# Performance work log

Hardware: AMD Instinct MI355X
Metric: run time of the kernel (lower is better)

## Reference

```python
import jax, jax.numpy as jnp
import numpy as np

RADIUS = 0.25
NUM_NEIGHBORS = 32
POS_DIM = 24
STEM_C = 64
PATCH_C = 256
LN_EPS = 1e-5


def query_ball_point(radius, nsample, xyz, new_xyz):
    # xyz: [B,N,3], new_xyz: [B,S,3] -> idx [B,S,nsample] (PointNet++ ball query)
    N = xyz.shape[1]
    sqr = (jnp.sum(new_xyz ** 2, -1)[:, :, None]
           + jnp.sum(xyz ** 2, -1)[:, None, :]
           - 2.0 * jnp.einsum('bsd,bnd->bsn', new_xyz, xyz))  # [B,S,N]
    idx = jnp.broadcast_to(jnp.arange(N, dtype=jnp.int32), sqr.shape)
    idx = jnp.where(sqr > radius * radius, N, idx)
    idx = jnp.sort(idx, axis=-1)[..., :nsample]  # first nsample in-ball (by index order)
    first = idx[..., :1]
    idx = jnp.where(idx == N, first, idx)  # pad empty slots with first neighbor
    return idx


def index_points(points, idx):
    # points [B,N,C], idx [B,S,K] -> [B,S,K,C]
    return jax.vmap(lambda p, i: p[i])(points, idx)


def rel_pos_encoding(rel_xyz, dim=POS_DIM):
    # sinusoidal Fourier encoding of 3D offsets: 3 coords * 2 (sin,cos) * dim//6 freqs
    nf = dim // 6
    freqs = 2.0 ** jnp.arange(nf, dtype=rel_xyz.dtype)
    ang = rel_xyz[..., None] * freqs  # [...,3,nf]
    enc = jnp.concatenate([jnp.sin(ang), jnp.cos(ang)], axis=-1)  # [...,3,2nf]
    return enc.reshape(rel_xyz.shape[:-1] + (dim,))


def point_mlp(x, W, b, gamma, beta, activate):
    h = jnp.einsum('...i,io->...o', x, W) + b
    mu = jnp.mean(h, -1, keepdims=True)
    var = jnp.mean((h - mu) ** 2, -1, keepdims=True)
    h = (h - mu) * jax.lax.rsqrt(var + LN_EPS) * gamma + beta
    return jax.nn.gelu(h, approximate=False) if activate else h


def setup_inputs() -> dict:
    key = jax.random.key(0)
    ks = jax.random.split(key, 8)
    B, N, S = 8, 16384, 1024
    in_c = STEM_C + 3 + POS_DIM  # 91
    return {
        'xyz': jax.random.uniform(ks[0], (B, N, 3), dtype=jnp.float32),
        'point_feature': jax.random.normal(ks[1], (B, N, STEM_C), dtype=jnp.float32),
        'patch_center': jax.random.uniform(ks[2], (B, S, 3), dtype=jnp.float32),
        'W1': jax.random.normal(ks[3], (in_c, PATCH_C), dtype=jnp.float32) * 0.02,
        'b1': jnp.zeros((PATCH_C,), jnp.float32),
        'g1': jnp.ones((PATCH_C,), jnp.float32),
        'be1': jnp.zeros((PATCH_C,), jnp.float32),
        'W2': jax.random.normal(ks[4], (PATCH_C, PATCH_C), dtype=jnp.float32) * 0.02,
        'b2': jnp.zeros((PATCH_C,), jnp.float32),
        'g2': jnp.ones((PATCH_C,), jnp.float32),
        'be2': jnp.zeros((PATCH_C,), jnp.float32),
    }


def reference(xyz, point_feature, patch_center, W1, b1, g1, be1, W2, b2, g2, be2):
    neighbor_idx = query_ball_point(RADIUS, NUM_NEIGHBORS, xyz, patch_center)  # [B,S,K]
    grouped_xyz = index_points(xyz, neighbor_idx)              # [B,S,K,3]
    grouped_feature = index_points(point_feature, neighbor_idx)  # [B,S,K,C]
    relative_xyz = grouped_xyz - patch_center[:, :, None, :]
    relative_position = rel_pos_encoding(relative_xyz)         # [B,S,K,24]
    grouped_input = jnp.concatenate((grouped_feature, relative_xyz, relative_position), axis=-1)
    h = point_mlp(grouped_input, W1, b1, g1, be1, True)
    h = point_mlp(h, W2, b2, g2, be2, False)
    patch_feature = jnp.max(h, axis=2)                         # max over neighbors -> [B,S,PATCH_C]
    return patch_feature, neighbor_idx
```

## Files before the change

### kernel.cpp

```cpp
#include <hip/hip_runtime.h>
#include <math.h>

#define NPTS 16384
#define KN 32
#define C 256
#define NQ 8192
#define PF_ELEMS (NQ * C)

#define W1P_ELEMS (3 * 16 * 64 * 8)
#define W2P_ELEMS (8 * 16 * 64 * 8)

typedef _Float16 half8 __attribute__((ext_vector_type(8)));
typedef _Float16 half4v __attribute__((ext_vector_type(4)));
typedef float f32x4 __attribute__((ext_vector_type(4)));

__global__ void prep_w_kernel(const float* __restrict__ W1,
                              const float* __restrict__ W2,
                              _Float16* __restrict__ wp) {
    const int e = blockIdx.x * 256 + threadIdx.x;
    if (e < W1P_ELEMS) {
        const int j = e & 7, lane = (e >> 3) & 63, nt = (e >> 9) & 15, kt = e >> 13;
        const int k = kt * 32 + (lane >> 4) * 8 + j;
        const int n = nt * 16 + (lane & 15);
        wp[e] = (_Float16)((k < 91) ? W1[k * C + n] : 0.0f);
    } else {
        const int e2 = e - W1P_ELEMS;
        const int j = e2 & 7, lane = (e2 >> 3) & 63, nt = (e2 >> 9) & 15, kt = e2 >> 13;
        const int k = kt * 32 + (lane >> 4) * 8 + j;
        const int n = nt * 16 + (lane & 15);
        wp[e] = (_Float16)W2[k * C + n];
    }
}

__device__ __forceinline__ float gelu_tanh(float x) {
    const float t  = x * x;
    const float p2 = fmaf(t, 0.0713548162726f, 1.59576912161f);
    const float e  = __expf(x * p2);
    return x - x * __builtin_amdgcn_rcpf(e + 1.0f);
}

__global__ void __launch_bounds__(256, 5)
encoder_fused(const float* __restrict__ xyz,
              const float* __restrict__ pf,
              const float* __restrict__ ctr,
              const float* __restrict__ b1, const float* __restrict__ g1,
              const float* __restrict__ be1,
              const float* __restrict__ b2, const float* __restrict__ g2,
              const float* __restrict__ be2,
              const _Float16* __restrict__ w1p,
              const _Float16* __restrict__ w2p,
              float* __restrict__ out0,
              float* __restrict__ out1) {
    const int q = blockIdx.x;
    const int b = q >> 10;
    const int t = threadIdx.x;
    const int w = t >> 6;
    const int lane = t & 63;
    const int quad = lane >> 4;
    const int l15  = lane & 15;

    __shared__ __align__(16) unsigned char H16raw[KN * 264 * 2];
    __shared__ __align__(16) unsigned char Xsraw[KN * 104 * 2];
    __shared__ float lnp[4 * 256];
    __shared__ int nbr[KN];
    __shared__ int wcnt[4];

    _Float16 (*H16)[264] = (_Float16(*)[264])H16raw;
    _Float16 (*Xs)[104]  = (_Float16(*)[104])Xsraw;
    float* lng1  = lnp;        float* lnbe1 = lnp + 256;
    float* lng2  = lnp + 512;  float* lnbe2 = lnp + 768;

    lnp[t]       = g1[t];  lnp[256 + t] = be1[t];
    lnp[512 + t] = g2[t];  lnp[768 + t] = be2[t];

    const float* xb = xyz + (size_t)b * NPTS * 3;
    const float cx = ctr[q * 3 + 0];
    const float cy = ctr[q * 3 + 1];
    const float cz = ctr[q * 3 + 2];
    const float sc = __fadd_rn(__fadd_rn(__fmul_rn(cx, cx), __fmul_rn(cy, cy)),
                               __fmul_rn(cz, cz));

    int found = 0;
    for (int base = 0; base < NPTS; base += 256) {
        const int n = base + t;
        const float px = xb[n * 3 + 0];
        const float py = xb[n * 3 + 1];
        const float pz = xb[n * 3 + 2];
        const float sp = __fadd_rn(__fadd_rn(__fmul_rn(px, px), __fmul_rn(py, py)),
                                   __fmul_rn(pz, pz));
        const float dt = __fadd_rn(__fadd_rn(__fmul_rn(cx, px), __fmul_rn(cy, py)),
                                   __fmul_rn(cz, pz));
        const float sqr = __fsub_rn(__fadd_rn(sc, sp), __fmul_rn(2.0f, dt));
        const bool inball = (sqr <= 0.0625f);

        const unsigned long long m = __ballot(inball);
        if (lane == 0) wcnt[w] = (int)__popcll(m);
        __syncthreads();
        int pre = found;
        if (w > 0) pre += wcnt[0];
        if (w > 1) pre += wcnt[1];
        if (w > 2) pre += wcnt[2];
        const int tot = found + wcnt[0] + wcnt[1] + wcnt[2] + wcnt[3];
        const int pos = pre + (int)__popcll(m & ((1ull << lane) - 1ull));
        if (inball && pos < KN) nbr[pos] = n;
        found = tot;
        __syncthreads();
        if (found >= KN) break;
    }
    const int count = (found < KN) ? found : KN;
    const int first = (count > 0) ? nbr[0] : NPTS;

    if (t < KN)
        out1[(size_t)q * KN + t] = (float)((t < count) ? nbr[t] : first);

    {
        const int k  = t >> 3;
        const int tc = t & 7;
        const int nidx = (k < count) ? nbr[k] : first;
        const int n = (nidx < NPTS) ? nidx : NPTS - 1;
        const float rx = xb[n * 3 + 0] - cx;
        const float ry = xb[n * 3 + 1] - cy;
        const float rz = xb[n * 3 + 2] - cz;
        const float* pfr = pf + ((size_t)b * NPTS + n) * 64;

        const float4 f0 = *(const float4*)(pfr + tc * 8);
        const float4 f1 = *(const float4*)(pfr + tc * 8 + 4);
        half8 hv;
        hv[0] = (_Float16)f0.x; hv[1] = (_Float16)f0.y;
        hv[2] = (_Float16)f0.z; hv[3] = (_Float16)f0.w;
        hv[4] = (_Float16)f1.x; hv[5] = (_Float16)f1.y;
        hv[6] = (_Float16)f1.z; hv[7] = (_Float16)f1.w;
        *(half8*)&Xs[k][tc * 8] = hv;

        half4v ov;
        #pragma unroll
        for (int j = 0; j < 4; ++j) {
            const int c = 64 + tc * 4 + j;
            float v;
            if (c < 67) {
                v = (c == 64) ? rx : ((c == 65) ? ry : rz);
            } else if (c < 91) {
                const int jj = c - 67;
                const int d = jj >> 3;
                const int mm = jj & 7;
                const float f = (float)(1 << (mm & 3));
                const float r = (d == 0) ? rx : ((d == 1) ? ry : rz);
                v = (mm < 4) ? __sinf(r * f) : __cosf(r * f);
            } else {
                v = 0.0f;
            }
            ov[j] = (_Float16)v;
        }
        *(half4v*)&Xs[k][64 + tc * 4] = ov;
    }
    __syncthreads();

    {
        f32x4 acc[2][4];
        #pragma unroll
        for (int mt = 0; mt < 2; ++mt)
            #pragma unroll
            for (int nt = 0; nt < 4; ++nt)
                acc[mt][nt] = (f32x4){0.f, 0.f, 0.f, 0.f};

        #pragma unroll
        for (int kt = 0; kt < 3; ++kt) {
            const half8 a0 = *(const half8*)&Xs[l15][kt * 32 + quad * 8];
            const half8 a1 = *(const half8*)&Xs[16 + l15][kt * 32 + quad * 8];
            #pragma unroll
            for (int nt = 0; nt < 4; ++nt) {
                const int ntg = w * 4 + nt;
                const half8 bf = *(const half8*)&w1p[((kt * 16 + ntg) * 64 + lane) * 8];
                acc[0][nt] = __builtin_amdgcn_mfma_f32_16x16x32_f16(a0, bf, acc[0][nt], 0, 0, 0);
                acc[1][nt] = __builtin_amdgcn_mfma_f32_16x16x32_f16(a1, bf, acc[1][nt], 0, 0, 0);
            }
        }
        #pragma unroll
        for (int nt = 0; nt < 4; ++nt) {
            const int col = w * 64 + nt * 16 + l15;
            const float bb = b1[col];
            #pragma unroll
            for (int mt = 0; mt < 2; ++mt)
                #pragma unroll
                for (int r = 0; r < 4; ++r)
                    H16[mt * 16 + quad * 4 + r][col] = (_Float16)(acc[mt][nt][r] + bb);
        }
    }
    __syncthreads();

    const int row = t >> 3;
    const int p   = t & 7;

    {
        _Float16* r0 = &H16[row][16 * p];
        _Float16* r1 = &H16[row][128 + 16 * p];
        const half8 h0 = *(const half8*)r0;
        const half8 h1 = *(const half8*)(r0 + 8);
        const half8 h2 = *(const half8*)r1;
        const half8 h3 = *(const half8*)(r1 + 8);

        float s = 0.0f, s2 = 0.0f;
        #pragma unroll
        for (int e = 0; e < 8; ++e) {
            const float x0 = (float)h0[e], x1 = (float)h1[e];
            const float x2 = (float)h2[e], x3 = (float)h3[e];
            s += (x0 + x1) + (x2 + x3);
            s2 = fmaf(x0, x0, fmaf(x1, x1, fmaf(x2, x2, fmaf(x3, x3, s2))));
        }
        #pragma unroll
        for (int off = 1; off < 8; off <<= 1) {
            s  += __shfl_xor(s, off, 64);
            s2 += __shfl_xor(s2, off, 64);
        }
        const float mu  = s * (1.0f / 256.0f);
        const float var = fmaf(s2, 1.0f / 256.0f, -mu * mu);
        const float rs  = __builtin_amdgcn_rsqf(var + 1e-5f);

        const int c0 = 16 * p, c1 = 128 + 16 * p;
        half8 o0, o1, o2, o3;
        #pragma unroll
        for (int e = 0; e < 8; ++e) {
            o0[e] = (_Float16)gelu_tanh(fmaf(((float)h0[e] - mu) * rs, lng1[c0 + e],     lnbe1[c0 + e]));
            o1[e] = (_Float16)gelu_tanh(fmaf(((float)h1[e] - mu) * rs, lng1[c0 + 8 + e], lnbe1[c0 + 8 + e]));
            o2[e] = (_Float16)gelu_tanh(fmaf(((float)h2[e] - mu) * rs, lng1[c1 + e],     lnbe1[c1 + e]));
            o3[e] = (_Float16)gelu_tanh(fmaf(((float)h3[e] - mu) * rs, lng1[c1 + 8 + e], lnbe1[c1 + 8 + e]));
        }
        *(half8*)r0       = o0;
        *(half8*)(r0 + 8) = o1;
        *(half8*)r1       = o2;
        *(half8*)(r1 + 8) = o3;
    }
    __syncthreads();

    {
        f32x4 acc[2][4];
        #pragma unroll
        for (int mt = 0; mt < 2; ++mt)
            #pragma unroll
            for (int nt = 0; nt < 4; ++nt)
                acc[mt][nt] = (f32x4){0.f, 0.f, 0.f, 0.f};

        #pragma unroll
        for (int kt = 0; kt < 8; ++kt) {
            const half8 a0 = *(const half8*)&H16[l15][kt * 32 + quad * 8];
            const half8 a1 = *(const half8*)&H16[16 + l15][kt * 32 + quad * 8];
            #pragma unroll
            for (int nt = 0; nt < 4; ++nt) {
                const int ntg = w * 4 + nt;
                const half8 bf = *(const half8*)&w2p[((kt * 16 + ntg) * 64 + lane) * 8];
                acc[0][nt] = __builtin_amdgcn_mfma_f32_16x16x32_f16(a0, bf, acc[0][nt], 0, 0, 0);
                acc[1][nt] = __builtin_amdgcn_mfma_f32_16x16x32_f16(a1, bf, acc[1][nt], 0, 0, 0);
            }
        }
        __syncthreads();
        #pragma unroll
        for (int nt = 0; nt < 4; ++nt) {
            const int col = w * 64 + nt * 16 + l15;
            const float bb = b2[col];
            #pragma unroll
            for (int mt = 0; mt < 2; ++mt)
                #pragma unroll
                for (int r = 0; r < 4; ++r)
                    H16[mt * 16 + quad * 4 + r][col] = (_Float16)(acc[mt][nt][r] + bb);
        }
    }
    __syncthreads();

    {
        _Float16* r0 = &H16[row][16 * p];
        _Float16* r1 = &H16[row][128 + 16 * p];
        const half8 h0 = *(const half8*)r0;
        const half8 h1 = *(const half8*)(r0 + 8);
        const half8 h2 = *(const half8*)r1;
        const half8 h3 = *(const half8*)(r1 + 8);

        float s = 0.0f, s2 = 0.0f;
        #pragma unroll
        for (int e = 0; e < 8; ++e) {
            const float x0 = (float)h0[e], x1 = (float)h1[e];
            const float x2 = (float)h2[e], x3 = (float)h3[e];
            s += (x0 + x1) + (x2 + x3);
            s2 = fmaf(x0, x0, fmaf(x1, x1, fmaf(x2, x2, fmaf(x3, x3, s2))));
        }
        #pragma unroll
        for (int off = 1; off < 8; off <<= 1) {
            s  += __shfl_xor(s, off, 64);
            s2 += __shfl_xor(s2, off, 64);
        }
        const float mu  = s * (1.0f / 256.0f);
        const float var = fmaf(s2, 1.0f / 256.0f, -mu * mu);
        const float rs  = __builtin_amdgcn_rsqf(var + 1e-5f);

        const int c0 = 16 * p, c1 = 128 + 16 * p;
        half8 o0, o1, o2, o3;
        #pragma unroll
        for (int e = 0; e < 8; ++e) {
            o0[e] = (_Float16)fmaf(((float)h0[e] - mu) * rs, lng2[c0 + e],     lnbe2[c0 + e]);
            o1[e] = (_Float16)fmaf(((float)h1[e] - mu) * rs, lng2[c0 + 8 + e], lnbe2[c0 + 8 + e]);
            o2[e] = (_Float16)fmaf(((float)h2[e] - mu) * rs, lng2[c1 + e],     lnbe2[c1 + e]);
            o3[e] = (_Float16)fmaf(((float)h3[e] - mu) * rs, lng2[c1 + 8 + e], lnbe2[c1 + 8 + e]);
        }
        *(half8*)r0       = o0;
        *(half8*)(r0 + 8) = o1;
        *(half8*)r1       = o2;
        *(half8*)(r1 + 8) = o3;
    }
    __syncthreads();

    {
        float m = -INFINITY;
        #pragma unroll
        for (int k = 0; k < KN; ++k)
            m = fmaxf(m, (float)H16[k][t]);
        out0[(size_t)q * C + t] = m;
    }
}

extern "C" void kernel_launch(void* const* d_in, const int* in_sizes, int n_in,
                              void* d_out, int out_size, void* d_ws, size_t ws_size,
                              hipStream_t stream) {
    const float* xyz = (const float*)d_in[0];
    const float* pf  = (const float*)d_in[1];
    const float* ctr = (const float*)d_in[2];
    const float* W1  = (const float*)d_in[3];
    const float* b1  = (const float*)d_in[4];
    const float* g1  = (const float*)d_in[5];
    const float* be1 = (const float*)d_in[6];
    const float* W2  = (const float*)d_in[7];
    const float* b2  = (const float*)d_in[8];
    const float* g2  = (const float*)d_in[9];
    const float* be2 = (const float*)d_in[10];

    float* out = (float*)d_out;
    _Float16* wp = (_Float16*)d_ws;

    prep_w_kernel<<<(W1P_ELEMS + W2P_ELEMS) / 256, 256, 0, stream>>>(W1, W2, wp);
    encoder_fused<<<NQ, 256, 0, stream>>>(xyz, pf, ctr,
                                          b1, g1, be1, b2, g2, be2,
                                          wp, wp + W1P_ELEMS,
                                          out, out + PF_ELEMS);
}
```

Measured before the change: 195.4 us.

## Swizzle H16 layout, packed fp16 LayerNorm math, double-buffered ball-query counts

The kernel XOR-swizzles the 16-byte column groups of the LDS hidden buffer so MFMA A-operand loads and row-wise LayerNorm accesses avoid bank conflicts. LayerNorm statistics now use fdot2 and the affine step uses packed half2 arithmetic, with gamma/beta kept as fp16 in LDS. The ball-query loop drops one barrier per iteration by alternating between two wave-count buffers. The final max-over-neighbors is done on half2 pairs by 128 threads, occupancy is raised to 6 blocks per SM, and prep_w switches to coalesced reads. Doing the normalization in fp16 adds rounding error.

```diff
diff --git a/kernel.cpp b/kernel.cpp
--- a/kernel.cpp
+++ b/kernel.cpp
@@ -9,27 +9,21 @@
 
 #define W1P_ELEMS (3 * 16 * 64 * 8)
 #define W2P_ELEMS (8 * 16 * 64 * 8)
+#define HSTR 264
 
 typedef _Float16 half8 __attribute__((ext_vector_type(8)));
 typedef _Float16 half4v __attribute__((ext_vector_type(4)));
+typedef _Float16 half2t __attribute__((ext_vector_type(2)));
 typedef float f32x4 __attribute__((ext_vector_type(4)));
 
-__global__ void prep_w_kernel(const float* __restrict__ W1,
-                              const float* __restrict__ W2,
-                              _Float16* __restrict__ wp) {
-    const int e = blockIdx.x * 256 + threadIdx.x;
-    if (e < W1P_ELEMS) {
-        const int j = e & 7, lane = (e >> 3) & 63, nt = (e >> 9) & 15, kt = e >> 13;
-        const int k = kt * 32 + (lane >> 4) * 8 + j;
-        const int n = nt * 16 + (lane & 15);
-        wp[e] = (_Float16)((k < 91) ? W1[k * C + n] : 0.0f);
-    } else {
-        const int e2 = e - W1P_ELEMS;
-        const int j = e2 & 7, lane = (e2 >> 3) & 63, nt = (e2 >> 9) & 15, kt = e2 >> 13;
-        const int k = kt * 32 + (lane >> 4) * 8 + j;
-        const int n = nt * 16 + (lane & 15);
-        wp[e] = (_Float16)W2[k * C + n];
-    }
+union H8u { half8 v; half2t h2[4]; };
+
+__device__ __forceinline__ float fdot2f(half2t a, half2t b, float c) {
+#if __has_builtin(__builtin_amdgcn_fdot2)
+    return __builtin_amdgcn_fdot2(a, b, c, false);
+#else
+    return fmaf((float)a[1], (float)b[1], fmaf((float)a[0], (float)b[0], c));
+#endif
 }
 
 __device__ __forceinline__ float gelu_tanh(float x) {
@@ -39,7 +33,59 @@
     return x - x * __builtin_amdgcn_rcpf(e + 1.0f);
 }
 
-__global__ void __launch_bounds__(256, 5)
+__device__ __forceinline__ void stat8(const H8u& u, half2t ones, float& s, float& s2) {
+    #pragma unroll
+    for (int j = 0; j < 4; ++j) {
+        s  = fdot2f(u.h2[j], ones, s);
+        s2 = fdot2f(u.h2[j], u.h2[j], s2);
+    }
+}
+
+__device__ __forceinline__ void norm_gelu8(H8u& u, const H8u& g, const H8u& be,
+                                           half2t rsh, half2t nmuh) {
+    #pragma unroll
+    for (int j = 0; j < 4; ++j) {
+        const half2t A = g.h2[j] * rsh;
+        const half2t B = A * nmuh + be.h2[j];
+        const half2t y = u.h2[j] * A + B;
+        half2t o;
+        o[0] = (_Float16)gelu_tanh((float)y[0]);
+        o[1] = (_Float16)gelu_tanh((float)y[1]);
+        u.h2[j] = o;
+    }
+}
+
+__device__ __forceinline__ void norm8(H8u& u, const H8u& g, const H8u& be,
+                                      half2t rsh, half2t nmuh) {
+    #pragma unroll
+    for (int j = 0; j < 4; ++j) {
+        const half2t A = g.h2[j] * rsh;
+        const half2t B = A * nmuh + be.h2[j];
+        u.h2[j] = u.h2[j] * A + B;
+    }
+}
+
+__global__ void prep_w_kernel(const float* __restrict__ W1,
+                              const float* __restrict__ W2,
+                              _Float16* __restrict__ wp) {
+    const int idx = blockIdx.x * 256 + threadIdx.x;
+    if (idx < 96 * 256) {
+        const int k = idx >> 8, n = idx & 255;
+        const float v = (k < 91) ? W1[k * 256 + n] : 0.0f;
+        const int kt = k >> 5, quad = (k >> 3) & 3, j = k & 7;
+        const int nt = n >> 4, l15 = n & 15;
+        wp[(((kt * 16 + nt) * 64) + quad * 16 + l15) * 8 + j] = (_Float16)v;
+    } else {
+        const int e = idx - 96 * 256;
+        const int k = e >> 8, n = e & 255;
+        const int kt = k >> 5, quad = (k >> 3) & 3, j = k & 7;
+        const int nt = n >> 4, l15 = n & 15;
+        wp[W1P_ELEMS + (((kt * 16 + nt) * 64) + quad * 16 + l15) * 8 + j] =
+            (_Float16)W2[k * 256 + n];
+    }
+}
+
+__global__ void __launch_bounds__(256, 6)
 encoder_fused(const float* __restrict__ xyz,
               const float* __restrict__ pf,
               const float* __restrict__ ctr,
@@ -59,19 +105,23 @@
     const int quad = lane >> 4;
     const int l15  = lane & 15;
 
-    __shared__ __align__(16) unsigned char H16raw[KN * 264 * 2];
+    __shared__ __align__(16) unsigned char H16raw[KN * HSTR * 2];
     __shared__ __align__(16) unsigned char Xsraw[KN * 104 * 2];
-    __shared__ float lnp[4 * 256];
+    __shared__ __align__(16) _Float16 lnph[4 * 256];
     __shared__ int nbr[KN];
-    __shared__ int wcnt[4];
-
-    _Float16 (*H16)[264] = (_Float16(*)[264])H16raw;
-    _Float16 (*Xs)[104]  = (_Float16(*)[104])Xsraw;
-    float* lng1  = lnp;        float* lnbe1 = lnp + 256;
-    float* lng2  = lnp + 512;  float* lnbe2 = lnp + 768;
-
-    lnp[t]       = g1[t];  lnp[256 + t] = be1[t];
-    lnp[512 + t] = g2[t];  lnp[768 + t] = be2[t];
+    __shared__ int wcnt[2][4];
+
+    _Float16 (*H16)[HSTR] = (_Float16(*)[HSTR])H16raw;
+    _Float16 (*Xs)[104]   = (_Float16(*)[104])Xsraw;
+    _Float16* g1h  = lnph;
+    _Float16* be1h = lnph + 256;
+    _Float16* g2h  = lnph + 512;
+    _Float16* be2h = lnph + 768;
+
+    lnph[t]       = (_Float16)g1[t];
+    lnph[256 + t] = (_Float16)be1[t];
+    lnph[512 + t] = (_Float16)g2[t];
+    lnph[768 + t] = (_Float16)be2[t];
 
     const float* xb = xyz + (size_t)b * NPTS * 3;
     const float cx = ctr[q * 3 + 0];
@@ -81,6 +131,7 @@
                                __fmul_rn(cz, cz));
 
     int found = 0;
+    int par = 0;
     for (int base = 0; base < NPTS; base += 256) {
         const int n = base + t;
         const float px = xb[n * 3 + 0];
@@ -94,19 +145,20 @@
         const bool inball = (sqr <= 0.0625f);
 
         const unsigned long long m = __ballot(inball);
-        if (lane == 0) wcnt[w] = (int)__popcll(m);
+        if (lane == 0) wcnt[par][w] = (int)__popcll(m);
         __syncthreads();
         int pre = found;
-        if (w > 0) pre += wcnt[0];
-        if (w > 1) pre += wcnt[1];
-        if (w > 2) pre += wcnt[2];
-        const int tot = found + wcnt[0] + wcnt[1] + wcnt[2] + wcnt[3];
+        if (w > 0) pre += wcnt[par][0];
+        if (w > 1) pre += wcnt[par][1];
+        if (w > 2) pre += wcnt[par][2];
+        const int tot = found + wcnt[par][0] + wcnt[par][1] + wcnt[par][2] + wcnt[par][3];
         const int pos = pre + (int)__popcll(m & ((1ull << lane) - 1ull));
         if (inball && pos < KN) nbr[pos] = n;
         found = tot;
-        __syncthreads();
+        par ^= 1;
         if (found >= KN) break;
     }
+    __syncthreads();
     const int count = (found < KN) ? found : KN;
     const int first = (count > 0) ? nbr[0] : NPTS;
 
@@ -155,58 +207,63 @@
     }
     __syncthreads();
 
-    {
-        f32x4 acc[2][4];
+    const int qx = (quad ^ (l15 >> 2)) * 8;
+
+    f32x4 acc[2][4];
+
+    #pragma unroll
+    for (int mt = 0; mt < 2; ++mt)
+        #pragma unroll
+        for (int nt = 0; nt < 4; ++nt)
+            acc[mt][nt] = (f32x4){0.f, 0.f, 0.f, 0.f};
+
+    #pragma unroll
+    for (int kt = 0; kt < 3; ++kt) {
+        const half8 a0 = *(const half8*)&Xs[l15][kt * 32 + quad * 8];
+        const half8 a1 = *(const half8*)&Xs[16 + l15][kt * 32 + quad * 8];
+        #pragma unroll
+        for (int nt = 0; nt < 4; ++nt) {
+            const int ntg = w * 4 + nt;
+            const half8 bf = *(const half8*)&w1p[((kt * 16 + ntg) * 64 + lane) * 8];
+            acc[0][nt] = __builtin_amdgcn_mfma_f32_16x16x32_f16(a0, bf, acc[0][nt], 0, 0, 0);
+            acc[1][nt] = __builtin_amdgcn_mfma_f32_16x16x32_f16(a1, bf, acc[1][nt], 0, 0, 0);
+        }
+    }
+    #pragma unroll
+    for (int nt = 0; nt < 4; ++nt) {
+        const int col  = w * 64 + nt * 16 + l15;
+        const int colp = col ^ (quad << 3);
+        const float bb = b1[col];
         #pragma unroll
         for (int mt = 0; mt < 2; ++mt)
             #pragma unroll
-            for (int nt = 0; nt < 4; ++nt)
-                acc[mt][nt] = (f32x4){0.f, 0.f, 0.f, 0.f};
-
-        #pragma unroll
-        for (int kt = 0; kt < 3; ++kt) {
-            const half8 a0 = *(const half8*)&Xs[l15][kt * 32 + quad * 8];
-            const half8 a1 = *(const half8*)&Xs[16 + l15][kt * 32 + quad * 8];
-            #pragma unroll
-            for (int nt = 0; nt < 4; ++nt) {
-                const int ntg = w * 4 + nt;
-                const half8 bf = *(const half8*)&w1p[((kt * 16 + ntg) * 64 + lane) * 8];
-                acc[0][nt] = __builtin_amdgcn_mfma_f32_16x16x32_f16(a0, bf, acc[0][nt], 0, 0, 0);
-                acc[1][nt] = __builtin_amdgcn_mfma_f32_16x16x32_f16(a1, bf, acc[1][nt], 0, 0, 0);
-            }
-        }
-        #pragma unroll
-        for (int nt = 0; nt < 4; ++nt) {
-            const int col = w * 64 + nt * 16 + l15;
-            const float bb = b1[col];
-            #pragma unroll
-            for (int mt = 0; mt < 2; ++mt)
-                #pragma unroll
-                for (int r = 0; r < 4; ++r)
-                    H16[mt * 16 + quad * 4 + r][col] = (_Float16)(acc[mt][nt][r] + bb);
-        }
-    }
-    __syncthreads();
-
-    const int row = t >> 3;
-    const int p   = t & 7;
+            for (int r = 0; r < 4; ++r)
+                H16[16 * mt + 4 * quad + r][colp] = (_Float16)(acc[mt][nt][r] + bb);
+    }
+    __syncthreads();
+
+    const int row  = t >> 3;
+    const int p    = t & 7;
+    const int qrow = (row >> 2) & 3;
+    _Float16* hb = &H16[row][0];
+    const int a0o = (( 2 * p    ) ^ qrow) << 3;
+    const int a1o = (( 2 * p + 1) ^ qrow) << 3;
+    const int a2o = ((16 + 2 * p) ^ qrow) << 3;
+    const int a3o = ((17 + 2 * p) ^ qrow) << 3;
+    half2t ones;
+    ones[0] = (_Float16)1.0f;
+    ones[1] = (_Float16)1.0f;
 
     {
-        _Float16* r0 = &H16[row][16 * p];
-        _Float16* r1 = &H16[row][128 + 16 * p];
-        const half8 h0 = *(const half8*)r0;
-        const half8 h1 = *(const half8*)(r0 + 8);
-        const half8 h2 = *(const half8*)r1;
-        const half8 h3 = *(const half8*)(r1 + 8);
+        H8u u0, u1, u2, u3;
+        u0.v = *(const half8*)(hb + a0o);
+        u1.v = *(const half8*)(hb + a1o);
+        u2.v = *(const half8*)(hb + a2o);
+        u3.v = *(const half8*)(hb + a3o);
 
         float s = 0.0f, s2 = 0.0f;
-        #pragma unroll
-        for (int e = 0; e < 8; ++e) {
-            const float x0 = (float)h0[e], x1 = (float)h1[e];
-            const float x2 = (float)h2[e], x3 = (float)h3[e];
-            s += (x0 + x1) + (x2 + x3);
-            s2 = fmaf(x0, x0, fmaf(x1, x1, fmaf(x2, x2, fmaf(x3, x3, s2))));
-        }
+        stat8(u0, ones, s, s2); stat8(u1, ones, s, s2);
+        stat8(u2, ones, s, s2); stat8(u3, ones, s, s2);
         #pragma unroll
         for (int off = 1; off < 8; off <<= 1) {
             s  += __shfl_xor(s, off, 64);
@@ -215,73 +272,70 @@
         const float mu  = s * (1.0f / 256.0f);
         const float var = fmaf(s2, 1.0f / 256.0f, -mu * mu);
         const float rs  = __builtin_amdgcn_rsqf(var + 1e-5f);
-
-        const int c0 = 16 * p, c1 = 128 + 16 * p;
-        half8 o0, o1, o2, o3;
-        #pragma unroll
-        for (int e = 0; e < 8; ++e) {
-            o0[e] = (_Float16)gelu_tanh(fmaf(((float)h0[e] - mu) * rs, lng1[c0 + e],     lnbe1[c0 + e]));
-            o1[e] = (_Float16)gelu_tanh(fmaf(((float)h1[e] - mu) * rs, lng1[c0 + 8 + e], lnbe1[c0 + 8 + e]));
-            o2[e] = (_Float16)gelu_tanh(fmaf(((float)h2[e] - mu) * rs, lng1[c1 + e],     lnbe1[c1 + e]));
-            o3[e] = (_Float16)gelu_tanh(fmaf(((float)h3[e] - mu) * rs, lng1[c1 + 8 + e], lnbe1[c1 + 8 + e]));
-        }
-        *(half8*)r0       = o0;
-        *(half8*)(r0 + 8) = o1;
-        *(half8*)r1       = o2;
-        *(half8*)(r1 + 8) = o3;
-    }
-    __syncthreads();
-
-    {
-        f32x4 acc[2][4];
+        half2t rsh, nmuh;
+        rsh[0]  = (_Float16)rs;    rsh[1]  = (_Float16)rs;
+        nmuh[0] = (_Float16)(-mu); nmuh[1] = (_Float16)(-mu);
+
+        H8u gA0, gA1, gB0, gB1, bA0, bA1, bB0, bB1;
+        gA0.v = *(const half8*)&g1h[16 * p];        bA0.v = *(const half8*)&be1h[16 * p];
+        gA1.v = *(const half8*)&g1h[16 * p + 8];    bA1.v = *(const half8*)&be1h[16 * p + 8];
+        gB0.v = *(const half8*)&g1h[128 + 16 * p];  bB0.v = *(const half8*)&be1h[128 + 16 * p];
+        gB1.v = *(const half8*)&g1h[136 + 16 * p];  bB1.v = *(const half8*)&be1h[136 + 16 * p];
+
+        norm_gelu8(u0, gA0, bA0, rsh, nmuh);
+        norm_gelu8(u1, gA1, bA1, rsh, nmuh);
+        norm_gelu8(u2, gB0, bB0, rsh, nmuh);
+        norm_gelu8(u3, gB1, bB1, rsh, nmuh);
+
+        *(half8*)(hb + a0o) = u0.v;
+        *(half8*)(hb + a1o) = u1.v;
+        *(half8*)(hb + a2o) = u2.v;
+        *(half8*)(hb + a3o) = u3.v;
+    }
+    __syncthreads();
+
+    #pragma unroll
+    for (int mt = 0; mt < 2; ++mt)
+        #pragma unroll
+        for (int nt = 0; nt < 4; ++nt)
+            acc[mt][nt] = (f32x4){0.f, 0.f, 0.f, 0.f};
+
+    #pragma unroll
+    for (int kt = 0; kt < 8; ++kt) {
+        const half8 a0 = *(const half8*)&H16[l15][kt * 32 + qx];
+        const half8 a1 = *(const half8*)&H16[16 + l15][kt * 32 + qx];
+        #pragma unroll
+        for (int nt = 0; nt < 4; ++nt) {
+            const int ntg = w * 4 + nt;
+            const half8 bf = *(const half8*)&w2p[((kt * 16 + ntg) * 64 + lane) * 8];
+            acc[0][nt] = __builtin_amdgcn_mfma_f32_16x16x32_f16(a0, bf, acc[0][nt], 0, 0, 0);
+            acc[1][nt] = __builtin_amdgcn_mfma_f32_16x16x32_f16(a1, bf, acc[1][nt], 0, 0, 0);
+        }
+    }
+    __syncthreads();
+    #pragma unroll
+    for (int nt = 0; nt < 4; ++nt) {
+        const int col  = w * 64 + nt * 16 + l15;
+        const int colp = col ^ (quad << 3);
+        const float bb = b2[col];
         #pragma unroll
         for (int mt = 0; mt < 2; ++mt)
             #pragma unroll
-            for (int nt = 0; nt < 4; ++nt)
-                acc[mt][nt] = (f32x4){0.f, 0.f, 0.f, 0.f};
-
-        #pragma unroll
-        for (int kt = 0; kt < 8; ++kt) {
-            const half8 a0 = *(const half8*)&H16[l15][kt * 32 + quad * 8];
-            const half8 a1 = *(const half8*)&H16[16 + l15][kt * 32 + quad * 8];
-            #pragma unroll
-            for (int nt = 0; nt < 4; ++nt) {
-                const int ntg = w * 4 + nt;
-                const half8 bf = *(const half8*)&w2p[((kt * 16 + ntg) * 64 + lane) * 8];
-                acc[0][nt] = __builtin_amdgcn_mfma_f32_16x16x32_f16(a0, bf, acc[0][nt], 0, 0, 0);
-                acc[1][nt] = __builtin_amdgcn_mfma_f32_16x16x32_f16(a1, bf, acc[1][nt], 0, 0, 0);
-            }
-        }
-        __syncthreads();
-        #pragma unroll
-        for (int nt = 0; nt < 4; ++nt) {
-            const int col = w * 64 + nt * 16 + l15;
-            const float bb = b2[col];
-            #pragma unroll
-            for (int mt = 0; mt < 2; ++mt)
-                #pragma unroll
-                for (int r = 0; r < 4; ++r)
-                    H16[mt * 16 + quad * 4 + r][col] = (_Float16)(acc[mt][nt][r] + bb);
-        }
+            for (int r = 0; r < 4; ++r)
+                H16[16 * mt + 4 * quad + r][colp] = (_Float16)(acc[mt][nt][r] + bb);
     }
     __syncthreads();
 
     {
-        _Float16* r0 = &H16[row][16 * p];
-        _Float16* r1 = &H16[row][128 + 16 * p];
-        const half8 h0 = *(const half8*)r0;
-        const half8 h1 = *(const half8*)(r0 + 8);
-        const half8 h2 = *(const half8*)r1;
-        const half8 h3 = *(const half8*)(r1 + 8);
+        H8u u0, u1, u2, u3;
+        u0.v = *(const half8*)(hb + a0o);
+        u1.v = *(const half8*)(hb + a1o);
+        u2.v = *(const half8*)(hb + a2o);
+        u3.v = *(const half8*)(hb + a3o);
 
         float s = 0.0f, s2 = 0.0f;
-        #pragma unroll
-        for (int e = 0; e < 8; ++e) {
-            const float x0 = (float)h0[e], x1 = (float)h1[e];
-            const float x2 = (float)h2[e], x3 = (float)h3[e];
-            s += (x0 + x1) + (x2 + x3);
-            s2 = fmaf(x0, x0, fmaf(x1, x1, fmaf(x2, x2, fmaf(x3, x3, s2))));
-        }
+        stat8(u0, ones, s, s2); stat8(u1, ones, s, s2);
+        stat8(u2, ones, s, s2); stat8(u3, ones, s, s2);
         #pragma unroll
         for (int off = 1; off < 8; off <<= 1) {
             s  += __shfl_xor(s, off, 64);
@@ -290,29 +344,42 @@
         const float mu  = s * (1.0f / 256.0f);
         const float var = fmaf(s2, 1.0f / 256.0f, -mu * mu);
         const float rs  = __builtin_amdgcn_rsqf(var + 1e-5f);
-
-        const int c0 = 16 * p, c1 = 128 + 16 * p;
-        half8 o0, o1, o2, o3;
-        #pragma unroll
-        for (int e = 0; e < 8; ++e) {
-            o0[e] = (_Float16)fmaf(((float)h0[e] - mu) * rs, lng2[c0 + e],     lnbe2[c0 + e]);
-            o1[e] = (_Float16)fmaf(((float)h1[e] - mu) * rs, lng2[c0 + 8 + e], lnbe2[c0 + 8 + e]);
-            o2[e] = (_Float16)fmaf(((float)h2[e] - mu) * rs, lng2[c1 + e],     lnbe2[c1 + e]);
-            o3[e] = (_Float16)fmaf(((float)h3[e] - mu) * rs, lng2[c1 + 8 + e], lnbe2[c1 + 8 + e]);
-        }
-        *(half8*)r0       = o0;
-        *(half8*)(r0 + 8) = o1;
-        *(half8*)r1       = o2;
-        *(half8*)(r1 + 8) = o3;
-    }
-    __syncthreads();
-
-    {
-        float m = -INFINITY;
-        #pragma unroll
-        for (int k = 0; k < KN; ++k)
-            m = fmaxf(m, (float)H16[k][t]);
-        out0[(size_t)q * C + t] = m;
+        half2t rsh, nmuh;
+        rsh[0]  = (_Float16)rs;    rsh[1]  = (_Float16)rs;
+        nmuh[0] = (_Float16)(-mu); nmuh[1] = (_Float16)(-mu);
+
+        H8u gA0, gA1, gB0, gB1, bA0, bA1, bB0, bB1;
+        gA0.v = *(const half8*)&g2h[16 * p];        bA0.v = *(const half8*)&be2h[16 * p];
+        gA1.v = *(const half8*)&g2h[16 * p + 8];    bA1.v = *(const half8*)&be2h[16 * p + 8];
+        gB0.v = *(const half8*)&g2h[128 + 16 * p];  bB0.v = *(const half8*)&be2h[128 + 16 * p];
+        gB1.v = *(const half8*)&g2h[136 + 16 * p];  bB1.v = *(const half8*)&be2h[136 + 16 * p];
+
+        norm8(u0, gA0, bA0, rsh, nmuh);
+        norm8(u1, gA1, bA1, rsh, nmuh);
+        norm8(u2, gB0, bB0, rsh, nmuh);
+        norm8(u3, gB1, bB1, rsh, nmuh);
+
+        *(half8*)(hb + a0o) = u0.v;
+        *(half8*)(hb + a1o) = u1.v;
+        *(half8*)(hb + a2o) = u2.v;
+        *(half8*)(hb + a3o) = u3.v;
+    }
+    __syncthreads();
+
+    if (t < 128) {
+        const _Float16* Hf = &H16[0][0];
+        const int c = t >> 2;
+        const int o = (2 * t) & 7;
+        half2t mx = *(const half2t*)(Hf + (c << 3) + o);
+        #pragma unroll
+        for (int r = 1; r < KN; ++r) {
+            const half2t v = *(const half2t*)(Hf + r * HSTR + ((c ^ ((r >> 2) & 3)) << 3) + o);
+            mx = __builtin_elementwise_max(mx, v);
+        }
+        float2 o2;
+        o2.x = (float)mx[0];
+        o2.y = (float)mx[1];
+        *(float2*)&out0[(size_t)q * C + 2 * t] = o2;
     }
 }
 
@@ -334,7 +401,7 @@
     float* out = (float*)d_out;
     _Float16* wp = (_Float16*)d_ws;
 
-    prep_w_kernel<<<(W1P_ELEMS + W2P_ELEMS) / 256, 256, 0, stream>>>(W1, W2, wp);
+    prep_w_kernel<<<(96 * 256 + 65536) / 256, 256, 0, stream>>>(W1, W2, wp);
     encoder_fused<<<NQ, 256, 0, stream>>>(xyz, pf, ctr,
                                           b1, g1, be1, b2, g2, be2,
                                           wp, wp + W1P_ELEMS,
```

Result: faster. 191.2 us (-2.1%).
